# Kernel tuning notes

Measured on AMD Instinct MI355X. Metric: run time of the kernel, lower is better.

## Reference

```python
import jax, jax.numpy as jnp
import numpy as np

B, DIN, H, NACT = 8192, 1025, 1024, 1026
NHEAD = 513  # npatches + STOP
K = 32       # kR = kS


def _make_seq(key, batch, n, k):
    k_idx, k_len = jax.random.split(key)
    # distinct indices per row: top-k of a random permutation
    perm = jnp.argsort(jax.random.uniform(k_idx, (batch, n)), axis=1)[:, :k]
    seq_len = jax.random.randint(k_len, (batch,), 1, k + 1).astype(jnp.int32)
    mask = jnp.arange(k)[None, :] < seq_len[:, None]
    seq_idx = jnp.where(mask, perm, -1).astype(jnp.int32)
    return seq_idx, seq_len


def setup_inputs() -> dict:
    key = jax.random.key(0)
    ks = jax.random.split(key, 8)
    state = jax.random.normal(ks[0], (B, DIN), dtype=jnp.float32)
    W0 = jax.random.normal(ks[1], (DIN, H), dtype=jnp.float32) * (2.0 / DIN) ** 0.5
    b0 = jnp.zeros((H,), jnp.float32)
    W1 = jax.random.normal(ks[2], (H, H), dtype=jnp.float32) * (2.0 / H) ** 0.5
    b1 = jnp.zeros((H,), jnp.float32)
    W2 = jax.random.normal(ks[3], (H, NACT), dtype=jnp.float32) * 0.01
    b2 = jnp.zeros((NACT,), jnp.float32)
    seq_idx_R, seq_len_R = _make_seq(ks[4], B, NHEAD, K)
    seq_idx_S, seq_len_S = _make_seq(ks[5], B, NHEAD, K)
    return {"state": state, "W0": W0, "b0": b0, "W1": W1, "b1": b1,
            "W2": W2, "b2": b2,
            "seq_idx_R": seq_idx_R, "seq_len_R": seq_len_R,
            "seq_idx_S": seq_idx_S, "seq_len_S": seq_len_S}


def _mlp(state, W0, b0, W1, b1, W2, b2):
    h = jax.nn.relu(state @ W0 + b0)
    h = jax.nn.relu(h @ W1 + b1)
    return h @ W2 + b2  # (B, NACT) logits


def _logprob_entropy_wo_replacement(logits, seq_idx, seq_len):
    # Faithful vectorized version of logprob_entropy_wo_replacement_batched.
    bsz, n = logits.shape
    col = jnp.arange(n)[None, :]
    neg_inf = jnp.float32(-jnp.inf)

    def step(carry, xs):
        remaining, logp, ent = carry          # (B,N) bool, (B,), (B,)
        t, idx_t = xs                          # scalar, (B,)
        active = t < seq_len                   # (B,)
        masked_logits = jnp.where(remaining, logits, neg_inf)
        lp = jax.nn.log_softmax(masked_logits, axis=-1)
        p = jnp.exp(lp)
        mp = jnp.where(remaining, p, 0.0)
        mlp_ = jnp.where(remaining, lp, 0.0)
        ent_step = -jnp.sum(mp * mlp_, axis=-1)
        ent = ent + jnp.where(active, ent_step, 0.0)
        valid = active & (idx_t >= 0)
        idx_safe = jnp.where(valid, idx_t, 0)
        g = jnp.take_along_axis(lp, idx_safe[:, None], axis=1)[:, 0]
        logp = logp + jnp.where(valid, g, 0.0)
        hit = (col == idx_safe[:, None]) & valid[:, None]
        remaining = remaining & ~hit
        return (remaining, logp, ent), None

    init = (jnp.ones((bsz, n), bool), jnp.zeros((bsz,), jnp.float32),
            jnp.zeros((bsz,), jnp.float32))
    ts = jnp.arange(seq_idx.shape[1], dtype=jnp.int32)
    (_, logp, ent), _ = jax.lax.scan(step, init, (ts, seq_idx.T))
    return logp, ent


def reference(state, W0, b0, W1, b1, W2, b2,
              seq_idx_R, seq_len_R, seq_idx_S, seq_len_S):
    x = _mlp(state, W0, b0, W1, b1, W2, b2)
    logpR, entR = _logprob_entropy_wo_replacement(x[:, :NHEAD], seq_idx_R, seq_len_R)
    logpS, entS = _logprob_entropy_wo_replacement(x[:, NHEAD:NHEAD + NHEAD], seq_idx_S, seq_len_S)
    # rows: [total logprob, total entropy] as in get_log_prob's (logpR+logpS, entR+entS)
    return jnp.stack([logpR + logpS, entR + entS], axis=0)  # (2, B)
```

## Files before the change

### kernel.cpp

```cpp
#include <hip/hip_runtime.h>
#include <cstdint>
#include <cstddef>

#define BATCH 8192
#define DIN   1025
#define HID   1024
#define NACT  1026
#define NHEAD 513
#define KSEL  32
#define KP0   1088
#define LGN   1024

typedef unsigned short u16;
typedef short bf16x8 __attribute__((ext_vector_type(8)));
typedef float f32x4 __attribute__((ext_vector_type(4)));

__device__ __forceinline__ u16 f2bf(float f) {
  unsigned u = __float_as_uint(f);
  u += 0x7fff + ((u >> 16) & 1);
  return (u16)(u >> 16);
}
__device__ __forceinline__ float bf2f(u16 h) {
  return __uint_as_float((unsigned)h << 16);
}

__device__ __forceinline__ void async_cp16(const u16* g, u16* l) {
  __builtin_amdgcn_global_load_lds((const __attribute__((address_space(1))) void*)g,
                                   (__attribute__((address_space(3))) void*)l,
                                   16, 0, 0);
}

__global__ __launch_bounds__(512) void k_cvt(const float* __restrict__ state,
    const float* __restrict__ W0, const float* __restrict__ W1,
    const float* __restrict__ W2,
    u16* __restrict__ As, u16* __restrict__ W0t, u16* __restrict__ W1t,
    u16* __restrict__ W2t, u16* __restrict__ W2c) {
  const int tid = threadIdx.x;
  const int b = blockIdx.x;
  {
    int i = b * 512 + tid;
    const int QPR = KP0 / 4;
    int r = i / QPR, c4 = (i - r * QPR) * 4;
    const float* src = state + (size_t)r * DIN + c4;
    ushort4 o;
    if (c4 + 3 < DIN) {
      o.x = f2bf(src[0]); o.y = f2bf(src[1]); o.z = f2bf(src[2]); o.w = f2bf(src[3]);
    } else {
      o.x = (c4 + 0 < DIN) ? f2bf(src[0]) : 0;
      o.y = (c4 + 1 < DIN) ? f2bf(src[1]) : 0;
      o.z = (c4 + 2 < DIN) ? f2bf(src[2]) : 0;
      o.w = (c4 + 3 < DIN) ? f2bf(src[3]) : 0;
    }
    *(ushort4*)(As + (size_t)r * KP0 + c4) = o;
  }
  if (b >= 3137) return;
  if (b == 3136) {
    for (int e = tid; e < 2048; e += 512) {
      int j = e >> 10, k = e & 1023;
      W2c[e] = f2bf(W2[(size_t)k * NACT + 1024 + j]);
    }
    return;
  }
  const float* W; u16* Wt; int K, ldW, Kp, tt = b;
  if (tt < 1088)      { W = W0; Wt = W0t; K = DIN; ldW = HID;  Kp = KP0; }
  else if (tt < 2112) { tt -= 1088; W = W1; Wt = W1t; K = HID; ldW = HID;  Kp = HID; }
  else                { tt -= 2112; W = W2; Wt = W2t; K = HID; ldW = NACT; Kp = HID; }
  int n0 = (tt & 31) * 32, k0 = (tt >> 5) * 32;
  __shared__ float tile[32][33];
  const int tx = tid & 31, ty = tid >> 5;
#pragma unroll
  for (int i = 0; i < 32; i += 16) {
    int k = k0 + ty + i;
    tile[ty + i][tx] = (k < K) ? W[(size_t)k * ldW + n0 + tx] : 0.f;
  }
  __syncthreads();
#pragma unroll
  for (int i = 0; i < 32; i += 16)
    Wt[(size_t)(n0 + ty + i) * Kp + k0 + tx] = f2bf(tile[tx][ty + i]);
}

template<bool RELU, int K>
__global__ __launch_bounds__(512, 2)
void gemm_bt(const u16* __restrict__ A, const u16* __restrict__ Bt,
             const float* __restrict__ bias, u16* __restrict__ Cout, int ldc)
{
  __shared__ __align__(16) u16 lds[24576];

  const int d     = blockIdx.x;
  const int m8    = d & 7;
  const int ntile = (d >> 3) & 3;
  const int mtile = ((d >> 5) << 3) | m8;
  const size_t bm = (size_t)mtile * 128;
  const size_t bn = (size_t)ntile * 256;

  const int tid  = threadIdx.x;
  const int wave = tid >> 6;
  const int lane = tid & 63;
  const int waveM = wave >> 2, waveN = wave & 3;
  const int lr = lane & 15, lq = lane >> 4;

  const int rowA  = tid >> 2;
  const int gA_   = (tid & 3) ^ ((rowA >> 1) & 3);
  const int rowB0 = tid >> 2;
  const int gB0_  = (tid & 3) ^ ((rowB0 >> 1) & 3);
  const int rowB1 = rowB0 + 128;
  const int gB1_  = (tid & 3) ^ ((rowB1 >> 1) & 3);
  const u16* gA  = A  + (bm + rowA)  * (size_t)K + gA_  * 8;
  const u16* gB0 = Bt + (bn + rowB0) * (size_t)K + gB0_ * 8;
  const u16* gB1 = Bt + (bn + rowB1) * (size_t)K + gB1_ * 8;
  u16* lA  = lds + wave * 512;
  u16* lB0 = lds + 4096 + wave * 512;
  u16* lB1 = lB0 + 4096;

  f32x4 acc[4][4] = {};

  const int s = lq ^ ((lr >> 1) & 3);
  const u16* pa = lds + (waveM * 64 + lr) * 32 + s * 8;
  const u16* pb = lds + 4096 + (waveN * 64 + lr) * 32 + s * 8;

  auto issue = [&](int k0, int buf) {
    const int o = buf * 12288;
    async_cp16(gA  + k0, lA  + o);
    async_cp16(gB0 + k0, lB0 + o);
    async_cp16(gB1 + k0, lB1 + o);
  };

  const int NIT = K / 32;
  issue(0, 0);
#pragma unroll 2
  for (int it = 0; it < NIT; ++it) {
    const int buf = it & 1;
    if (it + 1 < NIT) {
      issue((it + 1) * 32, buf ^ 1);
      asm volatile("s_waitcnt vmcnt(3)\n\ts_barrier" ::: "memory");
    } else {
      asm volatile("s_waitcnt vmcnt(0)\n\ts_barrier" ::: "memory");
    }

    bf16x8 af[4], bf[4];
    const u16* qa = pa + buf * 12288;
    const u16* qb = pb + buf * 12288;
#pragma unroll
    for (int t = 0; t < 4; ++t) {
      af[t] = *(const bf16x8*)(qa + t * 512);
      bf[t] = *(const bf16x8*)(qb + t * 512);
    }
#pragma unroll
    for (int tm = 0; tm < 4; ++tm)
#pragma unroll
      for (int tn = 0; tn < 4; ++tn)
        acc[tm][tn] = __builtin_amdgcn_mfma_f32_16x16x32_bf16(af[tm], bf[tn], acc[tm][tn], 0, 0, 0);

    asm volatile("s_waitcnt lgkmcnt(0)\n\ts_barrier" ::: "memory");
  }

#pragma unroll
  for (int tm = 0; tm < 4; ++tm) {
    size_t rw = bm + waveM * 64 + tm * 16 + lq * 4;
#pragma unroll
    for (int tn = 0; tn < 4; ++tn) {
      int col = (int)bn + waveN * 64 + tn * 16 + lr;
      float bv = bias[col];
#pragma unroll
      for (int r = 0; r < 4; ++r) {
        float v = acc[tm][tn][r] + bv;
        if (RELU) v = fmaxf(v, 0.f);
        Cout[(rw + r) * ldc + col] = f2bf(v);
      }
    }
  }
}

__global__ __launch_bounds__(512) void k_sample(const u16* __restrict__ lgts,
    const u16* __restrict__ h2, const u16* __restrict__ W2c,
    const float* __restrict__ b2,
    const int* __restrict__ idxR, const int* __restrict__ lenR,
    const int* __restrict__ idxS, const int* __restrict__ lenS,
    float* __restrict__ out) {
  __shared__ float shf[16];
  const int tid = threadIdx.x;
  const int w = tid >> 6, lane = tid & 63;
  const int grp = w & 1, pair = w >> 1;
  const int row = blockIdx.x * 4 + pair;
  const u16* base = lgts + (size_t)row * LGN + (grp ? NHEAD : 0);
  const int* sidx = (grp ? idxS : idxR) + (size_t)row * KSEL;
  const int slen  = (grp ? lenS : lenR)[row];

  float x1024 = 0.f, x1025 = 0.f;
  if (grp) {
    float d0 = 0.f, d1 = 0.f;
    const u16* hr  = h2 + (size_t)row * HID + lane * 16;
    const u16* w0p = W2c + lane * 16;
    const u16* w1p = W2c + 1024 + lane * 16;
#pragma unroll
    for (int j = 0; j < 16; ++j) {
      float h = bf2f(hr[j]);
      d0 += h * bf2f(w0p[j]);
      d1 += h * bf2f(w1p[j]);
    }
#pragma unroll
    for (int dd = 32; dd; dd >>= 1) { d0 += __shfl_xor(d0, dd, 64); d1 += __shfl_xor(d1, dd, 64); }
    x1024 = d0 + b2[1024];
    x1025 = d1 + b2[1025];
  }
  const int NHm = grp ? 511 : 513;

  float m = -3.4e38f;
  for (int i = lane; i < NHm; i += 64) m = fmaxf(m, bf2f(base[i]));
  if (grp) {
    if (lane == 63) m = fmaxf(m, x1024);
    if (lane == 0)  m = fmaxf(m, x1025);
  }
#pragma unroll
  for (int dd = 32; dd; dd >>= 1) m = fmaxf(m, __shfl_xor(m, dd, 64));

  float S = 0.f, T = 0.f;
  for (int i = lane; i < NHm; i += 64) {
    float xi = bf2f(base[i]);
    float e = __expf(xi - m);
    S += e; T += e * xi;
  }
  if (grp) {
    if (lane == 63) { float e = __expf(x1024 - m); S += e; T += e * x1024; }
    if (lane == 0)  { float e = __expf(x1025 - m); S += e; T += e * x1025; }
  }
#pragma unroll
  for (int dd = 32; dd; dd >>= 1) { S += __shfl_xor(S, dd, 64); T += __shfl_xor(T, dd, 64); }

  float e = 0.f, ex = 0.f, xt = 0.f;
  int active = (lane < KSEL) && (lane < slen);
  int valid = 0;
  if (active) {
    int id = sidx[lane];
    if (id >= 0) {
      valid = 1;
      if (grp && id >= 511) xt = (id == 511) ? x1024 : x1025;
      else                  xt = bf2f(base[id]);
      e  = __expf(xt - m);
      ex = e * xt;
    }
  }
  float pe = e, pex = ex;
#pragma unroll
  for (int dd = 1; dd < 32; dd <<= 1) {
    float qa = __shfl_up(pe, dd, 64);
    float qb = __shfl_up(pex, dd, 64);
    if (lane >= dd) { pe += qa; pex += qb; }
  }
  float lp = 0.f, en = 0.f;
  if (active) {
    float St = S - (pe - e);
    float Tt = T - (pex - ex);
    float logZ = m + __logf(St);
    en = logZ - Tt / St;
    if (valid) lp = xt - logZ;
  }
#pragma unroll
  for (int dd = 32; dd; dd >>= 1) { lp += __shfl_xor(lp, dd, 64); en += __shfl_xor(en, dd, 64); }

  if (lane == 0) { shf[w * 2] = lp; shf[w * 2 + 1] = en; }
  __syncthreads();
  if (lane == 0 && grp == 0) {
    out[row]         = shf[pair * 4] + shf[pair * 4 + 2];
    out[BATCH + row] = shf[pair * 4 + 1] + shf[pair * 4 + 3];
  }
}

extern "C" void kernel_launch(void* const* d_in, const int* in_sizes, int n_in,
                              void* d_out, int out_size, void* d_ws, size_t ws_size,
                              hipStream_t stream) {
  (void)in_sizes; (void)n_in; (void)out_size; (void)ws_size;
  const float* state = (const float*)d_in[0];
  const float* W0 = (const float*)d_in[1];
  const float* b0 = (const float*)d_in[2];
  const float* W1 = (const float*)d_in[3];
  const float* b1 = (const float*)d_in[4];
  const float* W2 = (const float*)d_in[5];
  const float* b2 = (const float*)d_in[6];
  const int* idxR = (const int*)d_in[7];
  const int* lenR = (const int*)d_in[8];
  const int* idxS = (const int*)d_in[9];
  const int* lenS = (const int*)d_in[10];
  float* out = (float*)d_out;

  char* ws = (char*)d_ws;
  size_t off = 0;
  auto alloc = [&](size_t bytes) -> char* {
    char* p = ws + off;
    off = (off + bytes + 255) & ~(size_t)255;
    return p;
  };
  u16* As   = (u16*)alloc((size_t)BATCH * KP0 * 2);
  u16* W0t  = (u16*)alloc((size_t)HID * KP0 * 2);
  u16* W1t  = (u16*)alloc((size_t)HID * HID * 2);
  u16* W2t  = (u16*)alloc((size_t)HID * LGN * 2);
  u16* W2c  = (u16*)alloc((size_t)2 * 1024 * 2);
  u16* h1   = (u16*)alloc((size_t)BATCH * HID * 2);
  u16* h2   = (u16*)alloc((size_t)BATCH * HID * 2);
  u16* lgts = (u16*)alloc((size_t)BATCH * LGN * 2);

  k_cvt<<<4352, 512, 0, stream>>>(state, W0, W1, W2, As, W0t, W1t, W2t, W2c);

  gemm_bt<true,  KP0><<<256, 512, 0, stream>>>(As, W0t, b0, h1,   HID);
  gemm_bt<true,  HID><<<256, 512, 0, stream>>>(h1, W1t, b1, h2,   HID);
  gemm_bt<false, HID><<<256, 512, 0, stream>>>(h2, W2t, b2, lgts, LGN);

  k_sample<<<2048, 512, 0, stream>>>(lgts, h2, W2c, b2, idxR, lenR, idxS, lenS, out);
}
```

Baseline: 194.4 us.

## Fuse fp32 state-to-bf16 conversion into first GEMM via async fp32 LDS loads

The separate pass that converted the fp32 state matrix into a padded bf16 buffer is removed. The first GEMM now streams fp32 state rows straight into LDS with 4-byte async loads and converts them to bf16 in registers before the MFMAs. The odd 1025th input column is handled by a rank-1 fix-up in the epilogue. This saves a full write and re-read of the activation matrix, but the GEMM now moves twice as many bytes for A, issues many small 4-byte async copies, and runs at occupancy 1 with a larger LDS tile.

```diff
diff --git a/kernel.cpp b/kernel.cpp
--- a/kernel.cpp
+++ b/kernel.cpp
@@ -29,31 +29,19 @@
                                    (__attribute__((address_space(3))) void*)l,
                                    16, 0, 0);
 }
-
-__global__ __launch_bounds__(512) void k_cvt(const float* __restrict__ state,
+__device__ __forceinline__ void async_cp4(const float* g, float* l) {
+  __builtin_amdgcn_global_load_lds((const __attribute__((address_space(1))) void*)g,
+                                   (__attribute__((address_space(3))) void*)l,
+                                   4, 0, 0);
+}
+
+__global__ __launch_bounds__(512) void k_wcvt(
     const float* __restrict__ W0, const float* __restrict__ W1,
     const float* __restrict__ W2,
-    u16* __restrict__ As, u16* __restrict__ W0t, u16* __restrict__ W1t,
+    u16* __restrict__ W0t, u16* __restrict__ W1t,
     u16* __restrict__ W2t, u16* __restrict__ W2c) {
   const int tid = threadIdx.x;
   const int b = blockIdx.x;
-  {
-    int i = b * 512 + tid;
-    const int QPR = KP0 / 4;
-    int r = i / QPR, c4 = (i - r * QPR) * 4;
-    const float* src = state + (size_t)r * DIN + c4;
-    ushort4 o;
-    if (c4 + 3 < DIN) {
-      o.x = f2bf(src[0]); o.y = f2bf(src[1]); o.z = f2bf(src[2]); o.w = f2bf(src[3]);
-    } else {
-      o.x = (c4 + 0 < DIN) ? f2bf(src[0]) : 0;
-      o.y = (c4 + 1 < DIN) ? f2bf(src[1]) : 0;
-      o.z = (c4 + 2 < DIN) ? f2bf(src[2]) : 0;
-      o.w = (c4 + 3 < DIN) ? f2bf(src[3]) : 0;
-    }
-    *(ushort4*)(As + (size_t)r * KP0 + c4) = o;
-  }
-  if (b >= 3137) return;
   if (b == 3136) {
     for (int e = tid; e < 2048; e += 512) {
       int j = e >> 10, k = e & 1023;
@@ -79,6 +67,120 @@
     Wt[(size_t)(n0 + ty + i) * Kp + k0 + tx] = f2bf(tile[tx][ty + i]);
 }
 
+__global__ __launch_bounds__(512, 1)
+void gemm1_f32a(const float* __restrict__ A, const u16* __restrict__ Bt,
+                const float* __restrict__ bias, u16* __restrict__ Cout)
+{
+  __shared__ __align__(16) u16 lds[32768];
+
+  const int d     = blockIdx.x;
+  const int ntile = (d >> 3) & 3;
+  const int mtile = ((d >> 5) << 3) | (d & 7);
+  const size_t bm = (size_t)mtile * 128;
+  const size_t bn = (size_t)ntile * 256;
+
+  const int tid  = threadIdx.x;
+  const int wave = tid >> 6;
+  const int lane = tid & 63;
+  const int waveM = wave >> 2, waveN = wave & 3;
+  const int lr = lane & 15, lq = lane >> 4;
+
+  const float* aSrc[8];
+#pragma unroll
+  for (int j = 0; j < 8; ++j) {
+    int dd = j * 512 + tid;
+    int row = dd >> 5, kslot = dd & 31;
+    int gk = ((((kslot >> 2) ^ (row & 7))) << 2) | (kslot & 3);
+    aSrc[j] = A + (bm + row) * (size_t)DIN + gk;
+  }
+  const int rowB0 = tid >> 2;
+  const int gB0_  = (tid & 3) ^ ((rowB0 >> 1) & 3);
+  const int rowB1 = rowB0 + 128;
+  const int gB1_  = (tid & 3) ^ ((rowB1 >> 1) & 3);
+  const u16* gB0 = Bt + (bn + rowB0) * (size_t)KP0 + gB0_ * 8;
+  const u16* gB1 = Bt + (bn + rowB1) * (size_t)KP0 + gB1_ * 8;
+
+  f32x4 acc[4][4] = {};
+
+  const int sB = lq ^ ((lr >> 1) & 3);
+
+  auto issue = [&](int k0, int buf) {
+    u16* base = lds + buf * 16384;
+    float* af = (float*)base;
+#pragma unroll
+    for (int j = 0; j < 8; ++j)
+      async_cp4(aSrc[j] + k0, af + j * 512 + wave * 64);
+    u16* bb = base + 8192;
+    async_cp16(gB0 + k0, bb + wave * 512);
+    async_cp16(gB1 + k0, bb + 4096 + wave * 512);
+  };
+
+  const int NIT = 32;
+  issue(0, 0);
+  for (int it = 0; it < NIT; ++it) {
+    const int buf = it & 1;
+    if (it + 1 < NIT) {
+      issue((it + 1) * 32, buf ^ 1);
+      asm volatile("s_waitcnt vmcnt(10)\n\ts_barrier" ::: "memory");
+    } else {
+      asm volatile("s_waitcnt vmcnt(0)\n\ts_barrier" ::: "memory");
+    }
+
+    const u16* base = lds + buf * 16384;
+    bf16x8 af[4], bf[4];
+#pragma unroll
+    for (int t = 0; t < 4; ++t) {
+      int row = waveM * 64 + t * 16 + lr;
+      int c0 = (2 * lq) ^ (row & 7);
+      int c1 = (2 * lq + 1) ^ (row & 7);
+      f32x4 fa0 = *(const f32x4*)(base + row * 64 + c0 * 8);
+      f32x4 fa1 = *(const f32x4*)(base + row * 64 + c1 * 8);
+      bf16x8 v;
+      v[0] = (short)f2bf(fa0[0]); v[1] = (short)f2bf(fa0[1]);
+      v[2] = (short)f2bf(fa0[2]); v[3] = (short)f2bf(fa0[3]);
+      v[4] = (short)f2bf(fa1[0]); v[5] = (short)f2bf(fa1[1]);
+      v[6] = (short)f2bf(fa1[2]); v[7] = (short)f2bf(fa1[3]);
+      af[t] = v;
+    }
+    const u16* pb = base + 8192 + (waveN * 64 + lr) * 32 + sB * 8;
+#pragma unroll
+    for (int t = 0; t < 4; ++t) bf[t] = *(const bf16x8*)(pb + t * 512);
+#pragma unroll
+    for (int tm = 0; tm < 4; ++tm)
+#pragma unroll
+      for (int tn = 0; tn < 4; ++tn)
+        acc[tm][tn] = __builtin_amdgcn_mfma_f32_16x16x32_bf16(af[tm], bf[tn], acc[tm][tn], 0, 0, 0);
+
+    asm volatile("s_waitcnt lgkmcnt(0)\n\ts_barrier" ::: "memory");
+  }
+
+  float afix[4][4], bfix[4];
+#pragma unroll
+  for (int tm = 0; tm < 4; ++tm)
+#pragma unroll
+    for (int r = 0; r < 4; ++r)
+      afix[tm][r] = A[(bm + waveM * 64 + tm * 16 + lq * 4 + r) * (size_t)DIN + 1024];
+#pragma unroll
+  for (int tn = 0; tn < 4; ++tn)
+    bfix[tn] = bf2f(Bt[(bn + waveN * 64 + tn * 16 + lr) * (size_t)KP0 + 1024]);
+
+#pragma unroll
+  for (int tm = 0; tm < 4; ++tm) {
+    size_t rw = bm + waveM * 64 + tm * 16 + lq * 4;
+#pragma unroll
+    for (int tn = 0; tn < 4; ++tn) {
+      int col = (int)bn + waveN * 64 + tn * 16 + lr;
+      float bv = bias[col];
+#pragma unroll
+      for (int r = 0; r < 4; ++r) {
+        float v = acc[tm][tn][r] + afix[tm][r] * bfix[tn] + bv;
+        v = fmaxf(v, 0.f);
+        Cout[(rw + r) * HID + col] = f2bf(v);
+      }
+    }
+  }
+}
+
 template<bool RELU, int K>
 __global__ __launch_bounds__(512, 2)
 void gemm_bt(const u16* __restrict__ A, const u16* __restrict__ Bt,
@@ -87,9 +189,8 @@
   __shared__ __align__(16) u16 lds[24576];
 
   const int d     = blockIdx.x;
-  const int m8    = d & 7;
   const int ntile = (d >> 3) & 3;
-  const int mtile = ((d >> 5) << 3) | m8;
+  const int mtile = ((d >> 5) << 3) | (d & 7);
   const size_t bm = (size_t)mtile * 128;
   const size_t bn = (size_t)ntile * 256;
 
@@ -290,7 +391,6 @@
     off = (off + bytes + 255) & ~(size_t)255;
     return p;
   };
-  u16* As   = (u16*)alloc((size_t)BATCH * KP0 * 2);
   u16* W0t  = (u16*)alloc((size_t)HID * KP0 * 2);
   u16* W1t  = (u16*)alloc((size_t)HID * HID * 2);
   u16* W2t  = (u16*)alloc((size_t)HID * LGN * 2);
@@ -299,11 +399,11 @@
   u16* h2   = (u16*)alloc((size_t)BATCH * HID * 2);
   u16* lgts = (u16*)alloc((size_t)BATCH * LGN * 2);
 
-  k_cvt<<<4352, 512, 0, stream>>>(state, W0, W1, W2, As, W0t, W1t, W2t, W2c);
-
-  gemm_bt<true,  KP0><<<256, 512, 0, stream>>>(As, W0t, b0, h1,   HID);
-  gemm_bt<true,  HID><<<256, 512, 0, stream>>>(h1, W1t, b1, h2,   HID);
-  gemm_bt<false, HID><<<256, 512, 0, stream>>>(h2, W2t, b2, lgts, LGN);
+  k_wcvt<<<3137, 512, 0, stream>>>(W0, W1, W2, W0t, W1t, W2t, W2c);
+
+  gemm1_f32a        <<<256, 512, 0, stream>>>(state, W0t, b0, h1);
+  gemm_bt<true, HID><<<256, 512, 0, stream>>>(h1, W1t, b1, h2,   HID);
+  gemm_bt<false,HID><<<256, 512, 0, stream>>>(h2, W2t, b2, lgts, LGN);
 
   k_sample<<<2048, 512, 0, stream>>>(lgts, h2, W2c, b2, idxR, lenR, idxS, lenS, out);
 }
```

Result: slower. 210.8 us (+8.4%).
